# Kernel tuning notes

Measured on AMD Instinct MI355X. Metric: run time of the kernel, lower is better.

## Reference

```python
import jax, jax.numpy as jnp
import numpy as np

# dims: batch, seq, d_model, heads, experts, expert hidden, top-k
B, S, D, H, E, F, K = 8, 512, 768, 12, 8, 3072, 2
DH = D // H
TAU = 1.0  # routing temperature
EPS = 1e-5


def _ln(x, g, b):
    mu = jnp.mean(x, axis=-1, keepdims=True)
    var = jnp.var(x, axis=-1, keepdims=True)
    return (x - mu) * jax.lax.rsqrt(var + EPS) * g + b


def setup_inputs() -> dict:
    key = jax.random.key(0)
    ks = jax.random.split(key, 12)
    sd = 1.0 / np.sqrt(D)
    sf = 1.0 / np.sqrt(F)
    return {
        "x": jax.random.normal(ks[0], (B, S, D), jnp.float32),
        "wq": jax.random.normal(ks[1], (D, D), jnp.float32) * sd,
        "wk": jax.random.normal(ks[2], (D, D), jnp.float32) * sd,
        "wv": jax.random.normal(ks[3], (D, D), jnp.float32) * sd,
        "wo": jax.random.normal(ks[4], (D, D), jnp.float32) * sd,
        "ln1_g": jnp.ones((D,), jnp.float32),
        "ln1_b": jnp.zeros((D,), jnp.float32),
        "ln2_g": jnp.ones((D,), jnp.float32),
        "ln2_b": jnp.zeros((D,), jnp.float32),
        "gate_w": jax.random.normal(ks[5], (D, E), jnp.float32) * sd,
        "gate_b": jnp.zeros((E,), jnp.float32),
        "bias_e": jnp.zeros((E,), jnp.float32),  # bias_param: per-expert routing bias (selection only)
        "w1": jax.random.normal(ks[6], (E, D, F), jnp.float32) * sd,
        "b1": jnp.zeros((E, F), jnp.float32),
        "w2": jax.random.normal(ks[7], (E, F, D), jnp.float32) * sf,
        "b2": jnp.zeros((E, D), jnp.float32),
    }


def reference(x, wq, wk, wv, wo, ln1_g, ln1_b, ln2_g, ln2_b,
              gate_w, gate_b, bias_e, w1, b1, w2, b2):
    # --- pre-LN multi-head self-attention + residual ---
    h = _ln(x, ln1_g, ln1_b)
    q = (h @ wq).reshape(B, S, H, DH)
    k = (h @ wk).reshape(B, S, H, DH)
    v = (h @ wv).reshape(B, S, H, DH)
    scores = jnp.einsum("bqhd,bkhd->bhqk", q, k) / np.sqrt(DH).astype(np.float32)
    attn = jax.nn.softmax(scores, axis=-1)
    o = jnp.einsum("bhqk,bkhd->bqhd", attn, v).reshape(B, S, D) @ wo
    x = x + o

    # --- pre-LN top-k MoE + residual ---
    h = _ln(x, ln2_g, ln2_b).reshape(B * S, D)          # [T, D]
    logits = (h @ gate_w + gate_b) / TAU                # [T, E]
    sel_scores = logits + bias_e                        # bias used for selection only
    _, idx = jax.lax.top_k(sel_scores, K)               # [T, K]
    topk_logits = jnp.take_along_axis(logits, idx, axis=-1)
    gates = jax.nn.softmax(topk_logits, axis=-1)        # [T, K]
    # sparse combine weights [T, E]
    cw = jnp.zeros((B * S, E), x.dtype).at[jnp.arange(B * S)[:, None], idx].set(gates)
    mid = jax.nn.gelu(jnp.einsum("td,edf->tef", h, w1) + b1)   # [T, E, F]
    eout = jnp.einsum("tef,efd->ted", mid, w2) + b2            # [T, E, D]
    y = jnp.einsum("ted,te->td", eout, cw).reshape(B, S, D)
    return x + y
```

## Files before the change

### kernel.cpp

```cpp
#include <hip/hip_runtime.h>
#include <hip/hip_bf16.h>

using bf16 = __hip_bfloat16;

constexpr int NB = 8, NS = 512, ND = 768, NH = 12, NE = 8, NF = 3072, NT = 4096;
constexpr int HG = 4;
constexpr int NG = NH / HG;
constexpr int GW = HG * 64;
constexpr int FQ = 768;
constexpr int NP = NF / FQ;

typedef __attribute__((ext_vector_type(8))) short v8s;
typedef __attribute__((ext_vector_type(4))) float v4f;

__device__ __forceinline__ short f2bf(float v) {
    bf16 t = __float2bfloat16(v);
    return *reinterpret_cast<short*>(&t);
}
__device__ __forceinline__ float bf2f(short s) {
    bf16 t = *reinterpret_cast<bf16*>(&s);
    return __bfloat162float(t);
}

__launch_bounds__(256)
__global__ void ln_kernel(const float* __restrict__ x, const float* __restrict__ g,
                          const float* __restrict__ b, float* __restrict__ out) {
    const int t = blockIdx.x;
    const int tid = threadIdx.x;
    const float* xr = x + (size_t)t * ND;
    float v0 = xr[tid], v1 = xr[tid + 256], v2 = xr[tid + 512];
    float s = v0 + v1 + v2;
    float ss = v0 * v0 + v1 * v1 + v2 * v2;
#pragma unroll
    for (int off = 32; off >= 1; off >>= 1) {
        s += __shfl_xor(s, off);
        ss += __shfl_xor(ss, off);
    }
    __shared__ float rs[4], rss[4];
    const int wv = tid >> 6, ln = tid & 63;
    if (ln == 0) { rs[wv] = s; rss[wv] = ss; }
    __syncthreads();
    float S = rs[0] + rs[1] + rs[2] + rs[3];
    float SS = rss[0] + rss[1] + rss[2] + rss[3];
    float mu = S * (1.0f / ND);
    float var = SS * (1.0f / ND) - mu * mu;
    float r = rsqrtf(fmaxf(var, 0.f) + 1e-5f);
    float* orow = out + (size_t)t * ND;
    orow[tid]       = (v0 - mu) * r * g[tid]       + b[tid];
    orow[tid + 256] = (v1 - mu) * r * g[tid + 256] + b[tid + 256];
    orow[tid + 512] = (v2 - mu) * r * g[tid + 512] + b[tid + 512];
}

__device__ __forceinline__ void gemm3_core(const float* __restrict__ A, int lda,
                                           const float* __restrict__ Bsrc, int ldb,
                                           int Kd, int m0, v4f acc[4],
                                           short* Ah, short* Al, short* Bh, short* Bl) {
    const int tid = threadIdx.x, lane = tid & 63, wv = tid >> 6;
    const int qd = lane >> 4, l16 = lane & 15;
    const int ar = tid >> 2, ac = (tid & 3) * 8;
    const int bn = tid & 63, bk = (tid >> 6) * 8;
    const float* Arow = A + (size_t)(m0 + ar) * lda;
    for (int k0 = 0; k0 < Kd; k0 += 32) {
        {
            const float* asrc = Arow + k0 + ac;
            v8s ah, al;
#pragma unroll
            for (int j = 0; j < 8; j++) {
                float vv = asrc[j];
                short hi = f2bf(vv);
                ah[j] = hi;
                al[j] = f2bf(vv - bf2f(hi));
            }
            *(v8s*)&Ah[ar * 40 + ac] = ah;
            *(v8s*)&Al[ar * 40 + ac] = al;
        }
        {
            const float* bsrc = Bsrc + (size_t)(k0 + bk) * ldb + bn;
            v8s bh_, bl_;
#pragma unroll
            for (int j = 0; j < 8; j++) {
                float vv = bsrc[(size_t)j * ldb];
                short hi = f2bf(vv);
                bh_[j] = hi;
                bl_[j] = f2bf(vv - bf2f(hi));
            }
            *(v8s*)&Bh[bn * 40 + bk] = bh_;
            *(v8s*)&Bl[bn * 40 + bk] = bl_;
        }
        __syncthreads();
        v8s bhf = *(const v8s*)&Bh[(wv * 16 + l16) * 40 + qd * 8];
        v8s blf = *(const v8s*)&Bl[(wv * 16 + l16) * 40 + qd * 8];
#pragma unroll
        for (int t = 0; t < 4; t++) {
            v8s ahf = *(const v8s*)&Ah[(t * 16 + l16) * 40 + qd * 8];
            v8s alf = *(const v8s*)&Al[(t * 16 + l16) * 40 + qd * 8];
            acc[t] = __builtin_amdgcn_mfma_f32_16x16x32_bf16(ahf, bhf, acc[t], 0, 0, 0);
            acc[t] = __builtin_amdgcn_mfma_f32_16x16x32_bf16(ahf, blf, acc[t], 0, 0, 0);
            acc[t] = __builtin_amdgcn_mfma_f32_16x16x32_bf16(alf, bhf, acc[t], 0, 0, 0);
        }
        __syncthreads();
    }
}

template <int RES_MODE>
__launch_bounds__(256)
__global__ void sgemm3(const float* __restrict__ A, int lda, const float* __restrict__ Bw,
                       int ldb, int bcol0, const float* __restrict__ Res,
                       float* __restrict__ C, int ldc, int Kd) {
    __shared__ short Ah[64 * 40], Al[64 * 40], Bh[64 * 40], Bl[64 * 40];
    const int m0 = blockIdx.x * 64, n0 = blockIdx.y * 64;
    v4f acc[4] = {};
    gemm3_core(A, lda, Bw + bcol0 + n0, ldb, Kd, m0, acc, Ah, Al, Bh, Bl);
    const int tid = threadIdx.x, lane = tid & 63, wv = tid >> 6;
    const int qd = lane >> 4, l16 = lane & 15;
    const int c = n0 + wv * 16 + l16;
#pragma unroll
    for (int t = 0; t < 4; t++)
#pragma unroll
        for (int rg = 0; rg < 4; rg++) {
            const int r = m0 + t * 16 + qd * 4 + rg;
            size_t ci = (size_t)r * ldc + c;
            if (RES_MODE == 0) C[ci] = acc[t][rg];
            else if (RES_MODE == 1) C[ci] = Res[ci] + acc[t][rg];
            else C[ci] += acc[t][rg];
        }
}

__launch_bounds__(256)
__global__ void qkv3(const float* __restrict__ h, const float* __restrict__ wq,
                     const float* __restrict__ wk, const float* __restrict__ wv,
                     int bcol0, float* __restrict__ qo, float* __restrict__ ko,
                     float* __restrict__ vo) {
    __shared__ short Ah[64 * 40], Al[64 * 40], Bh[64 * 40], Bl[64 * 40];
    const int m0 = blockIdx.x * 64;
    const int ysel = blockIdx.y >> 2, ny = blockIdx.y & 3;
    const int n0 = ny * 64;
    const float* Bw = (ysel == 0) ? wq : (ysel == 1) ? wk : wv;
    float* C = (ysel == 0) ? qo : (ysel == 1) ? ko : vo;
    v4f acc[4] = {};
    gemm3_core(h, ND, Bw + bcol0 + n0, ND, ND, m0, acc, Ah, Al, Bh, Bl);
    const int tid = threadIdx.x, lane = tid & 63, wv_ = tid >> 6;
    const int qd = lane >> 4, l16 = lane & 15;
    const int c = n0 + wv_ * 16 + l16;
#pragma unroll
    for (int t = 0; t < 4; t++)
#pragma unroll
        for (int rg = 0; rg < 4; rg++) {
            const int r = m0 + t * 16 + qd * 4 + rg;
            C[(size_t)r * GW + c] = acc[t][rg];
        }
}

__launch_bounds__(512)
__global__ void attn_kernel(const float* __restrict__ q, const float* __restrict__ k,
                            const float* __restrict__ v, float* __restrict__ o) {
    __shared__ float qs[64][68];
    __shared__ float kp[64][68];
    __shared__ float vs[64][68];
    const int qt = blockIdx.x, hl = blockIdx.y, b = blockIdx.z;
    const int tid = threadIdx.x;
    const int half = tid >> 8, t8 = tid & 255;
    const int tx = t8 & 15, ty = t8 >> 4;
    const int hc = hl * 64;
    const int rb = half * 32 + ty;
    {
        const v4f* q4 = (const v4f*)(q + ((size_t)b * NS + qt * 64) * GW + hc);
#pragma unroll
        for (int i = 0; i < 2; i++) {
            int idx = tid + 512 * i;
            int r = idx >> 4, c4 = idx & 15;
            *(v4f*)&qs[r][c4 * 4] = q4[(size_t)r * (GW / 4) + c4];
        }
    }
    float oa[2][4] = {};
    float mi[2], li[2], al[2];
#pragma unroll
    for (int i = 0; i < 2; i++) { mi[i] = -1.0e30f; li[i] = 0.f; }
    for (int kt = 0; kt < NS / 64; kt++) {
        __syncthreads();
        {
            const v4f* k4 = (const v4f*)(k + ((size_t)b * NS + kt * 64) * GW + hc);
            const v4f* v4 = (const v4f*)(v + ((size_t)b * NS + kt * 64) * GW + hc);
#pragma unroll
            for (int i = 0; i < 2; i++) {
                int idx = tid + 512 * i;
                int r = idx >> 4, c4 = idx & 15;
                *(v4f*)&kp[r][c4 * 4] = k4[(size_t)r * (GW / 4) + c4];
                *(v4f*)&vs[r][c4 * 4] = v4[(size_t)r * (GW / 4) + c4];
            }
        }
        __syncthreads();
        float s[2][4] = {};
#pragma unroll
        for (int d0 = 0; d0 < 64; d0 += 4) {
            v4f av[2], bv[4];
#pragma unroll
            for (int i = 0; i < 2; i++) av[i] = *(const v4f*)&qs[rb + 16 * i][d0];
#pragma unroll
            for (int j = 0; j < 4; j++) bv[j] = *(const v4f*)&kp[tx + 16 * j][d0];
#pragma unroll
            for (int dd = 0; dd < 4; dd++)
#pragma unroll
                for (int i = 0; i < 2; i++)
#pragma unroll
                    for (int j = 0; j < 4; j++) s[i][j] += av[i][dd] * bv[j][dd];
        }
#pragma unroll
        for (int i = 0; i < 2; i++) {
#pragma unroll
            for (int j = 0; j < 4; j++) s[i][j] *= 0.125f;
            float mt = fmaxf(fmaxf(s[i][0], s[i][1]), fmaxf(s[i][2], s[i][3]));
#pragma unroll
            for (int off = 1; off < 16; off <<= 1) mt = fmaxf(mt, __shfl_xor(mt, off));
            float mn = fmaxf(mi[i], mt);
            al[i] = __expf(mi[i] - mn);
            mi[i] = mn;
            float rsum = 0.f;
#pragma unroll
            for (int j = 0; j < 4; j++) {
                s[i][j] = __expf(s[i][j] - mn);
                rsum += s[i][j];
            }
#pragma unroll
            for (int off = 1; off < 16; off <<= 1) rsum += __shfl_xor(rsum, off);
            li[i] = li[i] * al[i] + rsum;
        }
        __syncthreads();
#pragma unroll
        for (int i = 0; i < 2; i++)
#pragma unroll
            for (int j = 0; j < 4; j++) {
                kp[rb + 16 * i][tx + 16 * j] = s[i][j];
                oa[i][j] *= al[i];
            }
        __syncthreads();
#pragma unroll
        for (int d0 = 0; d0 < 64; d0 += 4) {
            v4f av[2];
#pragma unroll
            for (int i = 0; i < 2; i++) av[i] = *(const v4f*)&kp[rb + 16 * i][d0];
#pragma unroll
            for (int dd = 0; dd < 4; dd++) {
                float bb[4];
#pragma unroll
                for (int j = 0; j < 4; j++) bb[j] = vs[d0 + dd][tx + 16 * j];
#pragma unroll
                for (int i = 0; i < 2; i++)
#pragma unroll
                    for (int j = 0; j < 4; j++) oa[i][j] += av[i][dd] * bb[j];
            }
        }
    }
#pragma unroll
    for (int i = 0; i < 2; i++) {
        float inv = 1.0f / li[i];
#pragma unroll
        for (int j = 0; j < 4; j++)
            o[((size_t)b * NS + qt * 64 + rb + 16 * i) * GW + hc + tx + 16 * j] = oa[i][j] * inv;
    }
}

__launch_bounds__(256)
__global__ void route_kernel(const float* __restrict__ x1, const float* __restrict__ lg,
                             const float* __restrict__ lb, const float* __restrict__ gw,
                             const float* __restrict__ gb, const float* __restrict__ be,
                             int* __restrict__ cnt, int* __restrict__ list,
                             float* __restrict__ gates, bf16* __restrict__ h2) {
    const int lane = threadIdx.x & 63;
    const int t = blockIdx.x * 4 + (threadIdx.x >> 6);
    if (t >= NT) return;
    const float* xr = x1 + (size_t)t * ND;
    float xv[12];
    float s = 0.f, ss = 0.f;
#pragma unroll
    for (int i = 0; i < 12; i++) {
        xv[i] = xr[i * 64 + lane];
        s += xv[i];
        ss += xv[i] * xv[i];
    }
#pragma unroll
    for (int off = 32; off >= 1; off >>= 1) {
        s += __shfl_xor(s, off);
        ss += __shfl_xor(ss, off);
    }
    float mu = s * (1.0f / ND);
    float var = ss * (1.0f / ND) - mu * mu;
    float r = rsqrtf(fmaxf(var, 0.f) + 1e-5f);
    float le[NE];
#pragma unroll
    for (int e = 0; e < NE; e++) le[e] = 0.f;
    bf16* h2r = h2 + (size_t)t * ND;
#pragma unroll
    for (int i = 0; i < 12; i++) {
        int d = i * 64 + lane;
        float hn = (xv[i] - mu) * r * lg[d] + lb[d];
        h2r[d] = __float2bfloat16(hn);
#pragma unroll
        for (int e = 0; e < NE; e++) le[e] += hn * gw[d * NE + e];
    }
#pragma unroll
    for (int off = 1; off < 64; off <<= 1)
#pragma unroll
        for (int e = 0; e < NE; e++) le[e] += __shfl_xor(le[e], off);
    float m1 = -1.0e30f, m2 = -1.0e30f, l1 = 0.f, l2 = 0.f;
    int i1 = 0, i2 = 0;
#pragma unroll
    for (int e = 0; e < NE; e++) {
        float lv = le[e] + gb[e];
        float sv = lv + be[e];
        bool g1 = sv > m1;
        float pm1 = m1, pl1 = l1; int pi1 = i1;
        m1 = g1 ? sv : m1; l1 = g1 ? lv : l1; i1 = g1 ? e : i1;
        bool g2 = (!g1) && (sv > m2);
        m2 = g1 ? pm1 : (g2 ? sv : m2);
        l2 = g1 ? pl1 : (g2 ? lv : l2);
        i2 = g1 ? pi1 : (g2 ? e : i2);
    }
    float m = fmaxf(l1, l2);
    float e1 = __expf(l1 - m), e2 = __expf(l2 - m);
    float inv = 1.0f / (e1 + e2);
    if (lane == 0) {
        gates[t * 2 + 0] = e1 * inv;
        gates[t * 2 + 1] = e2 * inv;
        int p1 = atomicAdd(&cnt[i1], 1);
        if (p1 < NT) list[i1 * NT + p1] = t * 2 + 0;
        int p2 = atomicAdd(&cnt[i2], 1);
        if (p2 < NT) list[i2 * NT + p2] = t * 2 + 1;
    }
}

__launch_bounds__(256)
__global__ void moe_gemm1(const bf16* __restrict__ h2, const float* __restrict__ w1,
                          const float* __restrict__ b1, const int* __restrict__ cnt,
                          const int* __restrict__ list, bf16* __restrict__ mid, int fcol0) {
    const int e = blockIdx.x >> 6, tile = blockIdx.x & 63;
    const int n = min(cnt[e], NT);
    const int r0 = tile * 64;
    if (r0 >= n) return;
    const int f0 = blockIdx.y * 64;
    __shared__ int ent[64];
    __shared__ short As[64 * 40];
    __shared__ short Bs[64 * 40];
    const int tid = threadIdx.x;
    const int lane = tid & 63, wv = tid >> 6;
    const int qd = lane >> 4, l16 = lane & 15;
    if (tid < 64) {
        int en = (r0 + tid < n) ? list[e * NT + r0 + tid] : -1;
        if (en < 0 || en >= 2 * NT) en = -1;
        ent[tid] = en;
    }
    __syncthreads();
    v4f acc[4] = {};
    const float* w1e = w1 + (size_t)e * ND * NF + fcol0 + f0;
    const int ar = tid >> 2, ac = (tid & 3) * 8;
    const int bn = tid & 63, bk = (tid >> 6) * 8;
    const int aen = ent[ar];
    for (int k0 = 0; k0 < ND; k0 += 32) {
        v8s av = {};
        if (aen >= 0)
            av = *(const v8s*)((const short*)h2 + (size_t)(aen >> 1) * ND + k0 + ac);
        *(v8s*)&As[ar * 40 + ac] = av;
        {
            const float* src = w1e + (size_t)(k0 + bk) * NF + bn;
            v8s bv;
#pragma unroll
            for (int j = 0; j < 8; j++) bv[j] = f2bf(src[(size_t)j * NF]);
            *(v8s*)&Bs[bn * 40 + bk] = bv;
        }
        __syncthreads();
        v8s bfrag = *(const v8s*)&Bs[(wv * 16 + l16) * 40 + qd * 8];
#pragma unroll
        for (int t = 0; t < 4; t++) {
            v8s afrag = *(const v8s*)&As[(t * 16 + l16) * 40 + qd * 8];
            acc[t] = __builtin_amdgcn_mfma_f32_16x16x32_bf16(afrag, bfrag, acc[t], 0, 0, 0);
        }
        __syncthreads();
    }
    const int col = wv * 16 + l16;
    const float bias = b1[e * NF + fcol0 + f0 + col];
#pragma unroll
    for (int t = 0; t < 4; t++) {
#pragma unroll
        for (int rg = 0; rg < 4; rg++) {
            int en = ent[t * 16 + qd * 4 + rg];
            if (en < 0) continue;
            float xv = acc[t][rg] + bias;
            float th = tanhf(0.7978845608028654f * (xv + 0.044715f * xv * xv * xv));
            mid[((size_t)((en & 1) * NT) + (en >> 1)) * FQ + f0 + col] =
                __float2bfloat16(0.5f * xv * (1.0f + th));
        }
    }
}

__launch_bounds__(256)
__global__ void moe_gemm2(const bf16* __restrict__ mid, const float* __restrict__ w2,
                          const float* __restrict__ b2, const int* __restrict__ cnt,
                          const int* __restrict__ list, const float* __restrict__ gates,
                          float* __restrict__ x1, int fcol0, int add_b2) {
    const int e = blockIdx.x >> 6, tile = blockIdx.x & 63;
    const int n = min(cnt[e], NT);
    const int r0 = tile * 64;
    if (r0 >= n) return;
    const int d0 = blockIdx.y * 64;
    __shared__ int ent[64];
    __shared__ short As[64 * 40];
    __shared__ short Bs[64 * 40];
    const int tid = threadIdx.x;
    const int lane = tid & 63, wv = tid >> 6;
    const int qd = lane >> 4, l16 = lane & 15;
    if (tid < 64) {
        int en = (r0 + tid < n) ? list[e * NT + r0 + tid] : -1;
        if (en < 0 || en >= 2 * NT) en = -1;
        ent[tid] = en;
    }
    __syncthreads();
    v4f acc[4] = {};
    const float* w2e = w2 + (size_t)e * NF * ND + d0;
    const int ar = tid >> 2, ac = (tid & 3) * 8;
    const int bn = tid & 63, bk = (tid >> 6) * 8;
    const int aen = ent[ar];
    for (int k0 = 0; k0 < FQ; k0 += 32) {
        v8s av = {};
        if (aen >= 0)
            av = *(const v8s*)((const short*)mid +
                               ((size_t)((aen & 1) * NT) + (aen >> 1)) * FQ + k0 + ac);
        *(v8s*)&As[ar * 40 + ac] = av;
        {
            const float* src = w2e + (size_t)(fcol0 + k0 + bk) * ND + bn;
            v8s bv;
#pragma unroll
            for (int j = 0; j < 8; j++) bv[j] = f2bf(src[(size_t)j * ND]);
            *(v8s*)&Bs[bn * 40 + bk] = bv;
        }
        __syncthreads();
        v8s bfrag = *(const v8s*)&Bs[(wv * 16 + l16) * 40 + qd * 8];
#pragma unroll
        for (int t = 0; t < 4; t++) {
            v8s afrag = *(const v8s*)&As[(t * 16 + l16) * 40 + qd * 8];
            acc[t] = __builtin_amdgcn_mfma_f32_16x16x32_bf16(afrag, bfrag, acc[t], 0, 0, 0);
        }
        __syncthreads();
    }
    const int col = wv * 16 + l16;
    const float bias = add_b2 ? b2[e * ND + d0 + col] : 0.f;
#pragma unroll
    for (int t = 0; t < 4; t++) {
#pragma unroll
        for (int rg = 0; rg < 4; rg++) {
            int en = ent[t * 16 + qd * 4 + rg];
            if (en < 0) continue;
            float g = gates[en];
            atomicAdd(&x1[(size_t)(en >> 1) * ND + d0 + col], g * (acc[t][rg] + bias));
        }
    }
}

__launch_bounds__(256)
__global__ void final_kernel(const float* __restrict__ x1, float* __restrict__ out) {
    int i = blockIdx.x * 256 + threadIdx.x;
    out[i] = x1[i];
}

extern "C" void kernel_launch(void* const* d_in, const int* in_sizes, int n_in,
                              void* d_out, int out_size, void* d_ws, size_t ws_size,
                              hipStream_t stream) {
    const float* x    = (const float*)d_in[0];
    const float* wq   = (const float*)d_in[1];
    const float* wk   = (const float*)d_in[2];
    const float* wvp  = (const float*)d_in[3];
    const float* wo   = (const float*)d_in[4];
    const float* ln1g = (const float*)d_in[5];
    const float* ln1b = (const float*)d_in[6];
    const float* ln2g = (const float*)d_in[7];
    const float* ln2b = (const float*)d_in[8];
    const float* gw   = (const float*)d_in[9];
    const float* gb   = (const float*)d_in[10];
    const float* be   = (const float*)d_in[11];
    const float* w1   = (const float*)d_in[12];
    const float* b1   = (const float*)d_in[13];
    const float* w2   = (const float*)d_in[14];
    const float* b2   = (const float*)d_in[15];
    float* out = (float*)d_out;

    const size_t TDn = (size_t)NT * ND;
    const size_t TGn = (size_t)NT * GW;
    float* W = (float*)d_ws;
    int*   cnt   = (int*)W;
    int*   list  = cnt + NE;
    float* gates = (float*)(list + NE * NT);
    float* x1 = W + 41216;
    float* h  = x1 + TDn;
    float* R0 = h + TDn;
    float* q  = R0;
    float* k  = R0 + TGn;
    float* v  = R0 + 2 * TGn;
    float* og = R0 + 3 * TGn;
    bf16*  h2  = (bf16*)h;
    bf16*  mid = (bf16*)R0;

    hipMemsetAsync(cnt, 0, NE * sizeof(int), stream);

    ln_kernel<<<NT, 256, 0, stream>>>(x, ln1g, ln1b, h);
    for (int g = 0; g < NG; g++) {
        qkv3<<<dim3(NT / 64, 12), 256, 0, stream>>>(h, wq, wk, wvp, g * GW, q, k, v);
        attn_kernel<<<dim3(NS / 64, HG, NB), 512, 0, stream>>>(q, k, v, og);
        if (g == 0)
            sgemm3<1><<<dim3(NT / 64, ND / 64), 256, 0, stream>>>(
                og, GW, wo + (size_t)g * GW * ND, ND, 0, x, x1, ND, GW);
        else
            sgemm3<2><<<dim3(NT / 64, ND / 64), 256, 0, stream>>>(
                og, GW, wo + (size_t)g * GW * ND, ND, 0, nullptr, x1, ND, GW);
    }
    route_kernel<<<NT / 4, 256, 0, stream>>>(x1, ln2g, ln2b, gw, gb, be, cnt, list,
                                             gates, h2);
    for (int p = 0; p < NP; p++) {
        int fcol0 = p * FQ;
        moe_gemm1<<<dim3(NE * (NT / 64), FQ / 64), 256, 0, stream>>>(
            h2, w1, b1, cnt, list, mid, fcol0);
        moe_gemm2<<<dim3(NE * (NT / 64), ND / 64), 256, 0, stream>>>(
            mid, w2, b2, cnt, list, gates, x1, fcol0, p == 0 ? 1 : 0);
    }
    final_kernel<<<TDn / 256, 256, 0, stream>>>(x1, out);
}
```

Measured before the change: 1.198 ms.

## Halve attention query tile and batch routing atomics per block

The attention kernel now handles 32 query rows per block instead of 64, so each thread owns one row. This doubles the grid so the GPU's compute units are better filled. The cost is that each K/V tile is reloaded twice as often from global memory. The routing kernel now gathers each block's expert choices in shared memory and does one atomicAdd per expert per block, instead of two per token. The expert counters are also padded to separate cache lines, which cuts atomic contention.

```diff
diff --git a/kernel.cpp b/kernel.cpp
--- a/kernel.cpp
+++ b/kernel.cpp
@@ -9,6 +9,7 @@
 constexpr int GW = HG * 64;
 constexpr int FQ = 768;
 constexpr int NP = NF / FQ;
+constexpr int CS = 32;
 
 typedef __attribute__((ext_vector_type(8))) short v8s;
 typedef __attribute__((ext_vector_type(4))) float v4f;
@@ -154,28 +155,19 @@
 __launch_bounds__(512)
 __global__ void attn_kernel(const float* __restrict__ q, const float* __restrict__ k,
                             const float* __restrict__ v, float* __restrict__ o) {
-    __shared__ float qs[64][68];
+    __shared__ float qs[32][68];
     __shared__ float kp[64][68];
     __shared__ float vs[64][68];
     const int qt = blockIdx.x, hl = blockIdx.y, b = blockIdx.z;
     const int tid = threadIdx.x;
-    const int half = tid >> 8, t8 = tid & 255;
-    const int tx = t8 & 15, ty = t8 >> 4;
+    const int tx = tid & 15, rw = tid >> 4;
     const int hc = hl * 64;
-    const int rb = half * 32 + ty;
     {
-        const v4f* q4 = (const v4f*)(q + ((size_t)b * NS + qt * 64) * GW + hc);
-#pragma unroll
-        for (int i = 0; i < 2; i++) {
-            int idx = tid + 512 * i;
-            int r = idx >> 4, c4 = idx & 15;
-            *(v4f*)&qs[r][c4 * 4] = q4[(size_t)r * (GW / 4) + c4];
-        }
-    }
-    float oa[2][4] = {};
-    float mi[2], li[2], al[2];
-#pragma unroll
-    for (int i = 0; i < 2; i++) { mi[i] = -1.0e30f; li[i] = 0.f; }
+        const v4f* q4 = (const v4f*)(q + ((size_t)b * NS + qt * 32) * GW + hc);
+        *(v4f*)&qs[rw][tx * 4] = q4[(size_t)rw * (GW / 4) + tx];
+    }
+    float oa[4] = {};
+    float mi = -1.0e30f, li = 0.f;
     for (int kt = 0; kt < NS / 64; kt++) {
         __syncthreads();
         {
@@ -190,74 +182,59 @@
             }
         }
         __syncthreads();
-        float s[2][4] = {};
+        float s[4] = {};
 #pragma unroll
         for (int d0 = 0; d0 < 64; d0 += 4) {
-            v4f av[2], bv[4];
-#pragma unroll
-            for (int i = 0; i < 2; i++) av[i] = *(const v4f*)&qs[rb + 16 * i][d0];
+            v4f av = *(const v4f*)&qs[rw][d0];
+            v4f bv[4];
 #pragma unroll
             for (int j = 0; j < 4; j++) bv[j] = *(const v4f*)&kp[tx + 16 * j][d0];
 #pragma unroll
             for (int dd = 0; dd < 4; dd++)
 #pragma unroll
-                for (int i = 0; i < 2; i++)
-#pragma unroll
-                    for (int j = 0; j < 4; j++) s[i][j] += av[i][dd] * bv[j][dd];
-        }
-#pragma unroll
-        for (int i = 0; i < 2; i++) {
-#pragma unroll
-            for (int j = 0; j < 4; j++) s[i][j] *= 0.125f;
-            float mt = fmaxf(fmaxf(s[i][0], s[i][1]), fmaxf(s[i][2], s[i][3]));
-#pragma unroll
-            for (int off = 1; off < 16; off <<= 1) mt = fmaxf(mt, __shfl_xor(mt, off));
-            float mn = fmaxf(mi[i], mt);
-            al[i] = __expf(mi[i] - mn);
-            mi[i] = mn;
-            float rsum = 0.f;
-#pragma unroll
-            for (int j = 0; j < 4; j++) {
-                s[i][j] = __expf(s[i][j] - mn);
-                rsum += s[i][j];
-            }
-#pragma unroll
-            for (int off = 1; off < 16; off <<= 1) rsum += __shfl_xor(rsum, off);
-            li[i] = li[i] * al[i] + rsum;
-        }
-        __syncthreads();
-#pragma unroll
-        for (int i = 0; i < 2; i++)
-#pragma unroll
-            for (int j = 0; j < 4; j++) {
-                kp[rb + 16 * i][tx + 16 * j] = s[i][j];
-                oa[i][j] *= al[i];
-            }
+                for (int j = 0; j < 4; j++) s[j] += av[dd] * bv[j][dd];
+        }
+#pragma unroll
+        for (int j = 0; j < 4; j++) s[j] *= 0.125f;
+        float mt = fmaxf(fmaxf(s[0], s[1]), fmaxf(s[2], s[3]));
+#pragma unroll
+        for (int off = 1; off < 16; off <<= 1) mt = fmaxf(mt, __shfl_xor(mt, off));
+        float mn = fmaxf(mi, mt);
+        float al = __expf(mi - mn);
+        mi = mn;
+        float rsum = 0.f;
+#pragma unroll
+        for (int j = 0; j < 4; j++) {
+            s[j] = __expf(s[j] - mn);
+            rsum += s[j];
+        }
+#pragma unroll
+        for (int off = 1; off < 16; off <<= 1) rsum += __shfl_xor(rsum, off);
+        li = li * al + rsum;
+        __syncthreads();
+#pragma unroll
+        for (int j = 0; j < 4; j++) {
+            kp[rw][tx + 16 * j] = s[j];
+            oa[j] *= al;
+        }
         __syncthreads();
 #pragma unroll
         for (int d0 = 0; d0 < 64; d0 += 4) {
-            v4f av[2];
-#pragma unroll
-            for (int i = 0; i < 2; i++) av[i] = *(const v4f*)&kp[rb + 16 * i][d0];
+            v4f av = *(const v4f*)&kp[rw][d0];
 #pragma unroll
             for (int dd = 0; dd < 4; dd++) {
                 float bb[4];
 #pragma unroll
                 for (int j = 0; j < 4; j++) bb[j] = vs[d0 + dd][tx + 16 * j];
 #pragma unroll
-                for (int i = 0; i < 2; i++)
-#pragma unroll
-                    for (int j = 0; j < 4; j++) oa[i][j] += av[i][dd] * bb[j];
+                for (int j = 0; j < 4; j++) oa[j] += av[dd] * bb[j];
             }
         }
     }
-#pragma unroll
-    for (int i = 0; i < 2; i++) {
-        float inv = 1.0f / li[i];
-#pragma unroll
-        for (int j = 0; j < 4; j++)
-            o[((size_t)b * NS + qt * 64 + rb + 16 * i) * GW + hc + tx + 16 * j] = oa[i][j] * inv;
-    }
+    float inv = 1.0f / li;
+#pragma unroll
+    for (int j = 0; j < 4; j++)
+        o[((size_t)b * NS + qt * 32 + rw) * GW + hc + tx + 16 * j] = oa[j] * inv;
 }
 
 __launch_bounds__(256)
@@ -266,9 +243,10 @@
                              const float* __restrict__ gb, const float* __restrict__ be,
                              int* __restrict__ cnt, int* __restrict__ list,
                              float* __restrict__ gates, bf16* __restrict__ h2) {
+    __shared__ int se[8], sent[8];
     const int lane = threadIdx.x & 63;
-    const int t = blockIdx.x * 4 + (threadIdx.x >> 6);
-    if (t >= NT) return;
+    const int wv = threadIdx.x >> 6;
+    const int t = blockIdx.x * 4 + wv;
     const float* xr = x1 + (size_t)t * ND;
     float xv[12];
     float s = 0.f, ss = 0.f;
@@ -322,10 +300,24 @@
     if (lane == 0) {
         gates[t * 2 + 0] = e1 * inv;
         gates[t * 2 + 1] = e2 * inv;
-        int p1 = atomicAdd(&cnt[i1], 1);
-        if (p1 < NT) list[i1 * NT + p1] = t * 2 + 0;
-        int p2 = atomicAdd(&cnt[i2], 1);
-        if (p2 < NT) list[i2 * NT + p2] = t * 2 + 1;
+        se[wv * 2]       = i1; sent[wv * 2]       = t * 2;
+        se[wv * 2 + 1]   = i2; sent[wv * 2 + 1]   = t * 2 + 1;
+    }
+    __syncthreads();
+    if (threadIdx.x < NE) {
+        const int e = threadIdx.x;
+        int c = 0;
+#pragma unroll
+        for (int sl = 0; sl < 8; sl++) c += (se[sl] == e) ? 1 : 0;
+        if (c) {
+            int p = atomicAdd(&cnt[e * CS], c);
+#pragma unroll
+            for (int sl = 0; sl < 8; sl++)
+                if (se[sl] == e) {
+                    if (p < NT) list[e * NT + p] = sent[sl];
+                    p++;
+                }
+        }
     }
 }
 
@@ -334,7 +326,7 @@
                           const float* __restrict__ b1, const int* __restrict__ cnt,
                           const int* __restrict__ list, bf16* __restrict__ mid, int fcol0) {
     const int e = blockIdx.x >> 6, tile = blockIdx.x & 63;
-    const int n = min(cnt[e], NT);
+    const int n = min(cnt[e * CS], NT);
     const int r0 = tile * 64;
     if (r0 >= n) return;
     const int f0 = blockIdx.y * 64;
@@ -398,7 +390,7 @@
                           const int* __restrict__ list, const float* __restrict__ gates,
                           float* __restrict__ x1, int fcol0, int add_b2) {
     const int e = blockIdx.x >> 6, tile = blockIdx.x & 63;
-    const int n = min(cnt[e], NT);
+    const int n = min(cnt[e * CS], NT);
     const int r0 = tile * 64;
     if (r0 >= n) return;
     const int d0 = blockIdx.y * 64;
@@ -486,7 +478,7 @@
     const size_t TGn = (size_t)NT * GW;
     float* W = (float*)d_ws;
     int*   cnt   = (int*)W;
-    int*   list  = cnt + NE;
+    int*   list  = cnt + NE * CS;
     float* gates = (float*)(list + NE * NT);
     float* x1 = W + 41216;
     float* h  = x1 + TDn;
@@ -498,12 +490,12 @@
     bf16*  h2  = (bf16*)h;
     bf16*  mid = (bf16*)R0;
 
-    hipMemsetAsync(cnt, 0, NE * sizeof(int), stream);
+    hipMemsetAsync(cnt, 0, NE * CS * sizeof(int), stream);
 
     ln_kernel<<<NT, 256, 0, stream>>>(x, ln1g, ln1b, h);
     for (int g = 0; g < NG; g++) {
         qkv3<<<dim3(NT / 64, 12), 256, 0, stream>>>(h, wq, wk, wvp, g * GW, q, k, v);
-        attn_kernel<<<dim3(NS / 64, HG, NB), 512, 0, stream>>>(q, k, v, og);
+        attn_kernel<<<dim3(NS / 32, HG, NB), 512, 0, stream>>>(q, k, v, og);
         if (g == 0)
             sgemm3<1><<<dim3(NT / 64, ND / 64), 256, 0, stream>>>(
                 og, GW, wo + (size_t)g * GW * ND, ND, 0, x, x1, ND, GW);
```

After: 1.164 ms. 2.8% less time.
